# Kernel tuning notes

Hardware: AMD Instinct MI355X
Metric: run time of the kernel (lower is better)

The kernel has to match this reference:

```python
import jax, jax.numpy as jnp
import numpy as np

B, C, HGT, WID = 4096, 64, 8, 8
NUM_HEADS, HEAD_DIM = 8, 8
LN_EPS = 1e-5


def _make_chess_bias(size=8):
    idx = np.arange(size * size)
    r, c = idx // size, idx % size
    dr = np.abs(r[:, None] - r[None, :])
    dc = np.abs(c[:, None] - c[None, :])
    dist = dr + dc
    diag = dr == dc
    bias = np.where(dist == 0, 0.1, np.where(dist <= 2, 0.05, np.where(diag, 0.03, 0.0)))
    return jnp.asarray(bias, dtype=jnp.float32)


def setup_inputs() -> dict:
    key = jax.random.key(0)
    k = jax.random.split(key, 4)
    E = C
    return {
        "x": jax.random.normal(k[0], (B, C, HGT, WID), dtype=jnp.float32),
        "pos_embed": jax.random.normal(k[1], (1, C, HGT, WID), dtype=jnp.float32),
        "ln_gamma": jnp.ones((E,), dtype=jnp.float32),
        "ln_beta": jnp.zeros((E,), dtype=jnp.float32),
        "qkv_w": jax.random.normal(k[2], (3 * E, E), dtype=jnp.float32) / np.sqrt(E),
        "qkv_b": jnp.zeros((3 * E,), dtype=jnp.float32),
        "out_w": jax.random.normal(k[3], (E, E), dtype=jnp.float32) / np.sqrt(E),
        "out_b": jnp.zeros((E,), dtype=jnp.float32),
        "chess_bias": _make_chess_bias(8),
        "stage": 1,
    }


def reference(x, pos_embed, ln_gamma, ln_beta, qkv_w, qkv_b, out_w, out_b, chess_bias, stage):
    # stage is fixed (=1); params above are the stage-1 params.
    x = x + pos_embed                                   # [B, C, H, W]
    b, c, h, w = x.shape
    x_flat = x.reshape(b, c, h * w).transpose(0, 2, 1)  # [B, S, E], S = H*W
    # LayerNorm over embed dim
    mu = jnp.mean(x_flat, axis=-1, keepdims=True)
    var = jnp.var(x_flat, axis=-1, keepdims=True)
    x_norm = (x_flat - mu) * jax.lax.rsqrt(var + LN_EPS) * ln_gamma + ln_beta
    # QKV projection (torch Linear: y = x W^T + b)
    qkv = x_norm @ qkv_w.T + qkv_b                      # [B, S, 3E]
    s = h * w
    qkv = qkv.reshape(b, s, 3, NUM_HEADS, HEAD_DIM)
    q = qkv[:, :, 0].transpose(0, 2, 1, 3)              # [B, H, S, D]
    k = qkv[:, :, 1].transpose(0, 2, 1, 3)
    v = qkv[:, :, 2].transpose(0, 2, 1, 3)
    scores = jnp.einsum("bhsd,bhtd->bhst", q, k) * (HEAD_DIM ** -0.5)
    scores = scores + chess_bias[None, None, :, :]
    attn = jax.nn.softmax(scores, axis=-1)              # dropout = identity (eval)
    out = jnp.einsum("bhst,bhtd->bhsd", attn, v)        # [B, H, S, D]
    out = out.transpose(0, 2, 1, 3).reshape(b, s, c)    # [B, S, E]
    attn_out = out @ out_w.T + out_b
    x_out = x_flat + attn_out                           # residual
    return x_out.transpose(0, 2, 1).reshape(b, c, h, w)
```

## Files before the change

kernel.cpp:

```cpp
#include <hip/hip_runtime.h>
#include <stdint.h>


typedef __attribute__((ext_vector_type(8))) __bf16 bfrag;
typedef __attribute__((ext_vector_type(4))) __bf16 bf4;
typedef __attribute__((ext_vector_type(4))) float f32x4;

#define MFMA16(a, b, c) __builtin_amdgcn_mfma_f32_16x16x32_bf16((a), (b), (c), 0, 0, 0)

static __device__ __forceinline__ bfrag bsplat(float v) {
  bfrag z;
#pragma unroll
  for (int i = 0; i < 8; i++) z[i] = (__bf16)v;
  return z;
}

static __device__ __forceinline__ bfrag cvt8(const float* __restrict__ p) {
  float4 a = *(const float4*)p, b = *(const float4*)(p + 4);
  bfrag r;
  r[0] = (__bf16)a.x; r[1] = (__bf16)a.y; r[2] = (__bf16)a.z; r[3] = (__bf16)a.w;
  r[4] = (__bf16)b.x; r[5] = (__bf16)b.y; r[6] = (__bf16)b.z; r[7] = (__bf16)b.w;
  return r;
}

__global__ __launch_bounds__(256, 3) void chess_attn_kernel(
    const float* __restrict__ xg,    const float* __restrict__ posg,
    const float* __restrict__ gam,   const float* __restrict__ bet,
    const float* __restrict__ qkvw,  const float* __restrict__ qkvb,
    const float* __restrict__ outw,  const float* __restrict__ outb,
    const float* __restrict__ biasg, float* __restrict__ outg) {
  __shared__ __attribute__((aligned(16))) __bf16 P1[2][64 * 136];
  __shared__ __attribute__((aligned(16))) __bf16 P2[2][64 * 72];

  const int tid = threadIdx.x, lane = tid & 63, w = tid >> 6;
  const int m = lane & 15, g = lane >> 4;
  const int b0 = blockIdx.x * 2;
  const float LN2I = 1.4426950408889634f;
  const float SCL2 = 0.35355339059327373f * 1.4426950408889634f;

  {
    const int s = tid >> 2, q = tid & 3;
    const float4* pg = (const float4*)(gam + q * 16);
    const float4* pb = (const float4*)(bet + q * 16);
    float4 g0 = pg[0], g1 = pg[1], g2 = pg[2], g3 = pg[3];
    float4 b0v = pb[0], b1 = pb[1], b2 = pb[2], b3 = pb[3];
    float gr[16] = {g0.x, g0.y, g0.z, g0.w, g1.x, g1.y, g1.z, g1.w,
                    g2.x, g2.y, g2.z, g2.w, g3.x, g3.y, g3.z, g3.w};
    float br[16] = {b0v.x, b0v.y, b0v.z, b0v.w, b1.x, b1.y, b1.z, b1.w,
                    b2.x, b2.y, b2.z, b2.w, b3.x, b3.y, b3.z, b3.w};
    const float* pp = posg + (size_t)(q * 16) * 64 + s;
    float pv[16];
#pragma unroll
    for (int i = 0; i < 16; i++) pv[i] = pp[i * 64];
#pragma unroll
    for (int it = 0; it < 2; it++) {
      const float* xb = xg + (size_t)(b0 + it) * 4096 + (size_t)(q * 16) * 64 + s;
      float xr[16];
#pragma unroll
      for (int i = 0; i < 16; i++) xr[i] = xb[i * 64] + pv[i];
      float sum = 0.f, ss = 0.f;
#pragma unroll
      for (int i = 0; i < 16; i++) { sum += xr[i]; ss = fmaf(xr[i], xr[i], ss); }
      sum += __shfl_xor(sum, 1); ss += __shfl_xor(ss, 1);
      sum += __shfl_xor(sum, 2); ss += __shfl_xor(ss, 2);
      const float mu = sum * 0.015625f;
      const float rs = __builtin_amdgcn_rsqf(ss * 0.015625f - mu * mu + 1e-5f);
      bfrag o0, o1;
#pragma unroll
      for (int i = 0; i < 8; i++) o0[i] = (__bf16)((xr[i] - mu) * rs * gr[i] + br[i]);
#pragma unroll
      for (int i = 0; i < 8; i++) o1[i] = (__bf16)((xr[8 + i] - mu) * rs * gr[8 + i] + br[8 + i]);
      *(bfrag*)&P2[it][s * 72 + q * 16] = o0;
      *(bfrag*)&P2[it][s * 72 + q * 16 + 8] = o1;
    }
  }
  __syncthreads();

  bfrag XF[2][4][2];
#pragma unroll
  for (int it = 0; it < 2; it++)
#pragma unroll
    for (int st = 0; st < 4; st++) {
      XF[it][st][0] = *(const bfrag*)&P2[it][(st * 16 + m) * 72 + g * 8];
      XF[it][st][1] = *(const bfrag*)&P2[it][(st * 16 + m) * 72 + 32 + g * 8];
    }
  __syncthreads();

  {
#pragma unroll
    for (int i = 0; i < 2; i++) {
      const int nt = w + 4 * i;
      bfrag AW0 = cvt8(qkvw + (size_t)(nt * 16 + m) * 64 + g * 8);
      bfrag AW1 = cvt8(qkvw + (size_t)(nt * 16 + m) * 64 + 32 + g * 8);
      float4 qb4 = *(const float4*)(qkvb + nt * 16 + g * 4);
      const float qs = (i == 0) ? SCL2 : 1.0f;
      const float qbx = qb4.x * qs, qby = qb4.y * qs;
      const float qbz = qb4.z * qs, qbw = qb4.w * qs;
#pragma unroll
      for (int it = 0; it < 2; it++)
#pragma unroll
        for (int st = 0; st < 4; st++) {
          f32x4 c = {0.f, 0.f, 0.f, 0.f};
          c = MFMA16(AW0, XF[it][st][0], c);
          c = MFMA16(AW1, XF[it][st][1], c);
          bf4 pk;
          pk[0] = (__bf16)fmaf(c[0], qs, qbx); pk[1] = (__bf16)fmaf(c[1], qs, qby);
          pk[2] = (__bf16)fmaf(c[2], qs, qbz); pk[3] = (__bf16)fmaf(c[3], qs, qbw);
          *(bf4*)&P1[it][(st * 16 + m) * 136 + nt * 16 + g * 4] = pk;
        }
    }
    {
      const int n = 128 + w * 16 + m;
      bfrag BV0 = cvt8(qkvw + (size_t)n * 64 + g * 8);
      bfrag BV1 = cvt8(qkvw + (size_t)n * 64 + 32 + g * 8);
      const float vb = qkvb[n];
#pragma unroll
      for (int it = 0; it < 2; it++)
#pragma unroll
        for (int st = 0; st < 4; st++) {
          f32x4 c = {0.f, 0.f, 0.f, 0.f};
          c = MFMA16(XF[it][st][0], BV0, c);
          c = MFMA16(XF[it][st][1], BV1, c);
          bf4 pk;
#pragma unroll
          for (int r = 0; r < 4; r++) pk[r] = (__bf16)(c[r] + vb);
          *(bf4*)&P2[it][(w * 16 + m) * 72 + st * 16 + g * 4] = pk;
        }
    }
  }

  const bfrag ZF  = bsplat(0.f);
  const bfrag ONE = bsplat(1.f);
  __bf16* PS = &P2[0][0];
  const int a7 = m & 7;
  const int rowoffA = (16 * w + a7) * 72 + (m >> 3) * 4608;
  const int rowoffB = rowoffA + 8 * 72;

  bfrag VA[2][2][2];
#pragma unroll
  for (int it = 0; it < 2; it++)
#pragma unroll
    for (int hl = 0; hl < 2; hl++)
#pragma unroll
      for (int kf = 0; kf < 2; kf++)
        VA[it][hl][kf] = (m < 8)
            ? *(const bfrag*)&P2[it][(16 * w + 8 * hl + m) * 72 + kf * 32 + g * 8]
            : ((m == 8) ? ONE : ZF);

#pragma unroll
  for (int hl = 0; hl < 2; hl++) {
    const int h8 = 16 * w + 8 * hl;
    bfrag KA[2][4];
#pragma unroll
    for (int it = 0; it < 2; it++)
#pragma unroll
      for (int tt = 0; tt < 4; tt++)
        KA[it][tt] = (lane < 16) ? *(const bfrag*)&P1[it][(tt * 16 + m) * 136 + 64 + h8] : ZF;
#pragma unroll
    for (int st = 0; st < 4; st++) {
      f32x4 binit[4];
#pragma unroll
      for (int tt = 0; tt < 4; tt++) {
        float4 bv = *(const float4*)(biasg + (size_t)(st * 16 + m) * 64 + tt * 16 + g * 4);
        binit[tt][0] = bv.x * LN2I; binit[tt][1] = bv.y * LN2I;
        binit[tt][2] = bv.z * LN2I; binit[tt][3] = bv.w * LN2I;
      }
#pragma unroll
      for (int it = 0; it < 2; it++) {
        const int rowoff = it ? rowoffB : rowoffA;
        bfrag QB = (lane < 16) ? *(const bfrag*)&P1[it][(st * 16 + m) * 136 + h8] : ZF;
        f32x4 sc[4];
#pragma unroll
        for (int tt = 0; tt < 4; tt++)
          sc[tt] = MFMA16(KA[it][tt], QB, binit[tt]);
#pragma unroll
        for (int tt = 0; tt < 4; tt++) {
          bf4 pr;
          pr[0] = (__bf16)__builtin_amdgcn_exp2f(sc[tt][0]);
          pr[1] = (__bf16)__builtin_amdgcn_exp2f(sc[tt][1]);
          pr[2] = (__bf16)__builtin_amdgcn_exp2f(sc[tt][2]);
          pr[3] = (__bf16)__builtin_amdgcn_exp2f(sc[tt][3]);
          *(bf4*)&PS[rowoff + tt * 16 + g * 4] = pr;
        }
        bfrag PB0 = *(const bfrag*)&PS[rowoff + g * 8];
        bfrag PB1 = *(const bfrag*)&PS[rowoff + 32 + g * 8];
        f32x4 oo = {0.f, 0.f, 0.f, 0.f};
        oo = MFMA16(VA[it][hl][0], PB0, oo);
        oo = MFMA16(VA[it][hl][1], PB1, oo);
        const float rsum = __builtin_amdgcn_rcpf(__shfl(oo[0], 32 + m));
        bf4 ov;
#pragma unroll
        for (int r = 0; r < 4; r++) ov[r] = (__bf16)(oo[r] * rsum);
        if (g < 2) *(bf4*)&P1[it][(st * 16 + m) * 136 + 64 + h8 + g * 4] = ov;
      }
    }
  }
  __syncthreads();

  {
    bfrag A0[2], A1[2];
#pragma unroll
    for (int it = 0; it < 2; it++) {
      A0[it] = *(const bfrag*)&P1[it][(w * 16 + m) * 136 + 64 + g * 8];
      A1[it] = *(const bfrag*)&P1[it][(w * 16 + m) * 136 + 96 + g * 8];
    }
    const int sbase = w * 16 + g * 4;
#pragma unroll
    for (int et = 0; et < 4; et++) {
      const int e = et * 16 + m;
      bfrag BW0 = cvt8(outw + (size_t)e * 64 + g * 8);
      bfrag BW1 = cvt8(outw + (size_t)e * 64 + 32 + g * 8);
      const float ob = outb[e];
      float4 pv = *(const float4*)(posg + (size_t)e * 64 + sbase);
#pragma unroll
      for (int it = 0; it < 2; it++) {
        const size_t xoff = (size_t)(b0 + it) * 4096;
        f32x4 c = {0.f, 0.f, 0.f, 0.f};
        c = MFMA16(A0[it], BW0, c);
        c = MFMA16(A1[it], BW1, c);
        float4 xv = *(const float4*)(xg + xoff + (size_t)e * 64 + sbase);
        float4 o;
        o.x = c[0] + ob + xv.x + pv.x;
        o.y = c[1] + ob + xv.y + pv.y;
        o.z = c[2] + ob + xv.z + pv.z;
        o.w = c[3] + ob + xv.w + pv.w;
        *(float4*)(outg + xoff + (size_t)e * 64 + sbase) = o;
      }
    }
  }
}

extern "C" void kernel_launch(void* const* d_in, const int* in_sizes, int n_in,
                              void* d_out, int out_size, void* d_ws, size_t ws_size,
                              hipStream_t stream) {
  const float* xg   = (const float*)d_in[0];
  const float* pos  = (const float*)d_in[1];
  const float* gam  = (const float*)d_in[2];
  const float* bet  = (const float*)d_in[3];
  const float* qkvw = (const float*)d_in[4];
  const float* qkvb = (const float*)d_in[5];
  const float* outw = (const float*)d_in[6];
  const float* outb = (const float*)d_in[7];
  const float* cb   = (const float*)d_in[8];
  float* out = (float*)d_out;
  const int B = in_sizes[0] / (64 * 64);
  hipLaunchKernelGGL(chess_attn_kernel, dim3(B / 2), dim3(256), 0, stream,
                     xg, pos, gam, bet, qkvw, qkvb, outw, outb, cb, out);
}
```

Before: 184.3 us.

## Software-pipeline attention PV step one iteration behind the score/exp step

```diff
diff --git a/kernel.cpp b/kernel.cpp
--- a/kernel.cpp
+++ b/kernel.cpp
@@ -167,12 +167,19 @@
       }
 #pragma unroll
       for (int it = 0; it < 2; it++) {
+        const int c = hl * 8 + st * 2 + it;
         const int rowoff = it ? rowoffB : rowoffA;
         bfrag QB = (lane < 16) ? *(const bfrag*)&P1[it][(st * 16 + m) * 136 + h8] : ZF;
         f32x4 sc[4];
 #pragma unroll
         for (int tt = 0; tt < 4; tt++)
           sc[tt] = MFMA16(KA[it][tt], QB, binit[tt]);
+        bfrag PB0p = ZF, PB1p = ZF;
+        if (c > 0) {
+          const int po = ((c - 1) & 1) ? rowoffB : rowoffA;
+          PB0p = *(const bfrag*)&PS[po + g * 8];
+          PB1p = *(const bfrag*)&PS[po + 32 + g * 8];
+        }
 #pragma unroll
         for (int tt = 0; tt < 4; tt++) {
           bf4 pr;
@@ -182,18 +189,33 @@
           pr[3] = (__bf16)__builtin_amdgcn_exp2f(sc[tt][3]);
           *(bf4*)&PS[rowoff + tt * 16 + g * 4] = pr;
         }
-        bfrag PB0 = *(const bfrag*)&PS[rowoff + g * 8];
-        bfrag PB1 = *(const bfrag*)&PS[rowoff + 32 + g * 8];
-        f32x4 oo = {0.f, 0.f, 0.f, 0.f};
-        oo = MFMA16(VA[it][hl][0], PB0, oo);
-        oo = MFMA16(VA[it][hl][1], PB1, oo);
-        const float rsum = __builtin_amdgcn_rcpf(__shfl(oo[0], 32 + m));
-        bf4 ov;
-#pragma unroll
-        for (int r = 0; r < 4; r++) ov[r] = (__bf16)(oo[r] * rsum);
-        if (g < 2) *(bf4*)&P1[it][(st * 16 + m) * 136 + 64 + h8 + g * 4] = ov;
+        if (c > 0) {
+          const int pc = c - 1;
+          const int pit = pc & 1, pst = (pc >> 1) & 3, phl = pc >> 3;
+          const int ph8 = 16 * w + 8 * phl;
+          f32x4 oo = {0.f, 0.f, 0.f, 0.f};
+          oo = MFMA16(VA[pit][phl][0], PB0p, oo);
+          oo = MFMA16(VA[pit][phl][1], PB1p, oo);
+          const float rsum = __builtin_amdgcn_rcpf(__shfl(oo[0], 32 + m));
+          bf4 ov;
+#pragma unroll
+          for (int r = 0; r < 4; r++) ov[r] = (__bf16)(oo[r] * rsum);
+          if (g < 2) *(bf4*)&P1[pit][(pst * 16 + m) * 136 + 64 + ph8 + g * 4] = ov;
+        }
       }
     }
+  }
+  {
+    bfrag PB0p = *(const bfrag*)&PS[rowoffB + g * 8];
+    bfrag PB1p = *(const bfrag*)&PS[rowoffB + 32 + g * 8];
+    f32x4 oo = {0.f, 0.f, 0.f, 0.f};
+    oo = MFMA16(VA[1][1][0], PB0p, oo);
+    oo = MFMA16(VA[1][1][1], PB1p, oo);
+    const float rsum = __builtin_amdgcn_rcpf(__shfl(oo[0], 32 + m));
+    bf4 ov;
+#pragma unroll
+    for (int r = 0; r < 4; r++) ov[r] = (__bf16)(oo[r] * rsum);
+    if (g < 2) *(bf4*)&P1[1][(3 * 16 + m) * 136 + 64 + (16 * w + 8) + g * 4] = ov;
   }
   __syncthreads();
 
```

After: 183.0 us. About the same (-0.7%).
